# Performance work log

Measured on AMD Instinct MI355X. Metric: run time of the kernel, lower is better.

## Reference

```python
import jax, jax.numpy as jnp
import numpy as np

D_MODEL = 2816
N_HEADS = 16
DH = 512
N_KV = 2
MAX_CTX = 8192
POS = 4095  # current decode position (0-indexed)
EPS = 1e-6
Q_DIM = N_HEADS * DH
KV_DIM = N_KV * DH
NEG_INF = -1e9


def setup_inputs() -> dict:
    key = jax.random.key(0)
    ks = jax.random.split(key, 8)
    x = jax.random.normal(ks[0], (1, 1, D_MODEL), jnp.float32)
    # Realistic RoPE angles at position POS (full head_dim rotation, half/half layout)
    inv_freq = 1.0 / (10000.0 ** (np.arange(0, DH, 2, dtype=np.float32) / DH))  # (DH/2,)
    ang = POS * inv_freq
    cos = jnp.asarray(np.concatenate([np.cos(ang), np.cos(ang)])[None, None, :], jnp.float32)  # (1,1,DH)
    sin = jnp.asarray(np.concatenate([np.sin(ang), np.sin(ang)])[None, None, :], jnp.float32)
    k_cache = jax.random.normal(ks[1], (1, N_KV, MAX_CTX, DH), jnp.float32) * 0.02
    v_cache = jax.random.normal(ks[2], (1, N_KV, MAX_CTX, DH), jnp.float32) * 0.02
    # causal decode mask: attend to [0, POS], -inf beyond
    pos_ids = jnp.arange(MAX_CTX)
    attn_mask = jnp.where(pos_ids <= POS, 0.0, NEG_INF).astype(jnp.float32).reshape(1, 1, 1, MAX_CTX)
    # one-hot write mask at current position
    kv_write_mask = jnp.zeros((1, 1, MAX_CTX, 1), jnp.float32).at[0, 0, POS, 0].set(1.0)
    Wq = jax.random.normal(ks[3], (Q_DIM, D_MODEL), jnp.float32) * 0.02
    Wk = jax.random.normal(ks[4], (KV_DIM, D_MODEL), jnp.float32) * 0.02
    Wo = jax.random.normal(ks[5], (D_MODEL, Q_DIM), jnp.float32) * 0.02
    q_gamma = jax.random.normal(ks[6], (DH,), jnp.float32) * 0.02  # stored as (gamma-1)
    k_gamma = jax.random.normal(ks[7], (DH,), jnp.float32) * 0.02
    return {"x": x, "cos": cos, "sin": sin, "k_cache": k_cache, "v_cache": v_cache,
            "attn_mask": attn_mask, "kv_write_mask": kv_write_mask,
            "Wq": Wq, "Wk": Wk, "Wo": Wo, "q_gamma": q_gamma, "k_gamma": k_gamma}


def _rmsnorm(x, w=None):
    v = jnp.mean(x * x, axis=-1, keepdims=True)
    x = x * jax.lax.rsqrt(v + EPS)
    return x if w is None else x * (1.0 + w)


def _rope(x, cos, sin):
    # x: (1,T,H,D); cos/sin: (1,T,D)
    c = cos[:, :, None, :]
    s = sin[:, :, None, :]
    d = x.shape[-1]
    x1, x2 = x[..., : d // 2], x[..., d // 2 :]
    rot = jnp.concatenate([-x2, x1], axis=-1)
    return x * c + rot * s


def reference(x, cos, sin, k_cache, v_cache, attn_mask, kv_write_mask, Wq, Wk, Wo, q_gamma, k_gamma):
    q_raw = (x @ Wq.T).reshape(1, 1, N_HEADS, DH)
    k_raw = (x @ Wk.T).reshape(1, 1, N_KV, DH)
    q = _rope(_rmsnorm(q_raw, q_gamma), cos, sin)
    k = _rope(_rmsnorm(k_raw, k_gamma), cos, sin)
    v = _rmsnorm(k_raw)  # unscaled norm, not rotated
    q = jnp.swapaxes(q, 1, 2)  # (1,H,1,D)
    k = jnp.swapaxes(k, 1, 2)  # (1,n_kv,1,D)
    v = jnp.swapaxes(v, 1, 2)
    k_new = k_cache + k * kv_write_mask  # broadcast write at current slot
    v_new = v_cache + v * kv_write_mask
    rep = N_HEADS // N_KV
    K = jnp.repeat(k_new, rep, axis=1)  # (1,H,S,D)
    V = jnp.repeat(v_new, rep, axis=1)
    scores = jnp.einsum("bhtd,bhsd->bhts", q, K) + attn_mask  # no 1/sqrt(d) scale, as in source
    w = jax.nn.softmax(scores.astype(jnp.float32), axis=-1).astype(q.dtype)
    ctx = jnp.einsum("bhts,bhsd->bhtd", w, V)  # (1,H,1,D)
    ctx = jnp.swapaxes(ctx, 1, 2).reshape(1, 1, Q_DIM)
    out = ctx @ Wo.T
    return (out, k_new, v_new)
```

## Files before the change

kernel.cpp:

```cpp
#include <hip/hip_runtime.h>
#include <math.h>

#define D_MODEL 2816
#define N_HEADS 16
#define DH      512
#define N_KV    2
#define MAX_CTX 8192
#define POS     4095
#define EPS     1e-6f
#define Q_DIM   8192
#define KV_DIM  1024
#define GROUP   8
#define NPOS    4096
#define PV_CHUNK  64
#define PV_NCHUNK 64


__device__ __forceinline__ float4 f4_mul(float4 a, float s) {
  return make_float4(a.x*s, a.y*s, a.z*s, a.w*s);
}
__device__ __forceinline__ float4 f4_mul4(float4 a, float4 b) {
  return make_float4(a.x*b.x, a.y*b.y, a.z*b.z, a.w*b.w);
}
__device__ __forceinline__ float4 f4_fma(float4 a, float4 b, float4 c) {
  return make_float4(fmaf(a.x,b.x,c.x), fmaf(a.y,b.y,c.y), fmaf(a.z,b.z,c.z), fmaf(a.w,b.w,c.w));
}
__device__ __forceinline__ float4 f4_fnma(float4 a, float4 b, float4 c) {
  return make_float4(fmaf(-a.x,b.x,c.x), fmaf(-a.y,b.y,c.y), fmaf(-a.z,b.z,c.z), fmaf(-a.w,b.w,c.w));
}
__device__ __forceinline__ float4 f4_add(float4 a, float4 b) {
  return make_float4(a.x+b.x, a.y+b.y, a.z+b.z, a.w+b.w);
}
__device__ __forceinline__ float f4_dot(float4 a, float4 b) {
  return a.x*b.x + a.y*b.y + a.z*b.z + a.w*b.w;
}
__device__ __forceinline__ float f4_ssq(float4 a) {
  return a.x*a.x + a.y*a.y + a.z*a.z + a.w*a.w;
}

__global__ __launch_bounds__(256) void k_qkv(const float* __restrict__ x,
    const float* __restrict__ Wq, const float* __restrict__ Wk,
    float* __restrict__ qraw, float* __restrict__ kraw) {
  int wid  = (blockIdx.x * blockDim.x + threadIdx.x) >> 6;
  int lane = threadIdx.x & 63;
  const float4* x4 = (const float4*)x;
  int row = wid;
  const float4* W4 = (row < Q_DIM)
      ? (const float4*)(Wq + (size_t)row * D_MODEL)
      : (const float4*)(Wk + (size_t)(row - Q_DIM) * D_MODEL);
  float acc0 = 0.f, acc1 = 0.f;
#pragma unroll
  for (int it = 0; it < D_MODEL / 256; ++it) {
    float4 w  = W4[it * 64 + lane];
    float4 xv = x4[it * 64 + lane];
    float d = f4_dot(w, xv);
    if (it & 1) acc1 += d; else acc0 += d;
  }
  float acc = acc0 + acc1;
#pragma unroll
  for (int m = 32; m; m >>= 1) acc += __shfl_xor(acc, m, 64);
  if (lane == 0) {
    if (row < Q_DIM) qraw[row] = acc;
    else             kraw[row - Q_DIM] = acc;
  }
}

__global__ __launch_bounds__(512) void k_copy_scores(
    const float* __restrict__ kc, const float* __restrict__ vc,
    const float* __restrict__ qraw, const float* __restrict__ kraw,
    const float* __restrict__ cosv, const float* __restrict__ sinv,
    const float* __restrict__ qg,   const float* __restrict__ kg,
    float* __restrict__ knew, float* __restrict__ vnew,
    float* __restrict__ scores) {
  __shared__ float4 lq[GROUP * DH / 4];
  __shared__ float4 kfin[DH / 4];
  __shared__ float4 vfin[DH / 4];
  int b = blockIdx.x;
  int g = b >> 10;
  int t = threadIdx.x;
  int wid = t >> 6, lane = t & 63;

  const float4* c4 = (const float4*)cosv;
  const float4* s4 = (const float4*)sinv;
  float4 c1 = c4[lane],      s1 = s4[lane];
  float4 c2 = c4[64 + lane], s2 = s4[64 + lane];

  {
    const float4* qr4 = (const float4*)(qraw + (size_t)(g * GROUP + wid) * DH);
    float4 a  = qr4[lane];
    float4 b2 = qr4[64 + lane];
    float ss = f4_ssq(a) + f4_ssq(b2);
#pragma unroll
    for (int m = 32; m; m >>= 1) ss += __shfl_xor(ss, m, 64);
    float scale = rsqrtf(ss * (1.f / (float)DH) + EPS);
    const float4* qg4 = (const float4*)qg;
    float4 ga = qg4[lane], gb = qg4[64 + lane];
    float4 na = f4_mul4(f4_mul(a,  scale), make_float4(1.f+ga.x,1.f+ga.y,1.f+ga.z,1.f+ga.w));
    float4 nb = f4_mul4(f4_mul(b2, scale), make_float4(1.f+gb.x,1.f+gb.y,1.f+gb.z,1.f+gb.w));
    lq[wid * 128 + lane]      = f4_fnma(nb, s1, f4_mul4(na, c1));
    lq[wid * 128 + 64 + lane] = f4_fma (na, s2, f4_mul4(nb, c2));
  }

  bool has_pos = ((b & 1023) == (POS >> 3));
  if (has_pos && wid == 0) {
    const float4* kr4 = (const float4*)(kraw + (size_t)g * DH);
    float4 a  = kr4[lane];
    float4 b2 = kr4[64 + lane];
    float ss = f4_ssq(a) + f4_ssq(b2);
#pragma unroll
    for (int m = 32; m; m >>= 1) ss += __shfl_xor(ss, m, 64);
    float scale = rsqrtf(ss * (1.f / (float)DH) + EPS);
    float4 va_ = f4_mul(a,  scale);
    float4 vb_ = f4_mul(b2, scale);
    const float4* kg4 = (const float4*)kg;
    float4 ga = kg4[lane], gb = kg4[64 + lane];
    float4 na = f4_mul4(va_, make_float4(1.f+ga.x,1.f+ga.y,1.f+ga.z,1.f+ga.w));
    float4 nb = f4_mul4(vb_, make_float4(1.f+gb.x,1.f+gb.y,1.f+gb.z,1.f+gb.w));
    kfin[lane]      = f4_fnma(nb, s1, f4_mul4(na, c1));
    kfin[64 + lane] = f4_fma (na, s2, f4_mul4(nb, c2));
    vfin[lane]      = va_;
    vfin[64 + lane] = vb_;
  }
  __syncthreads();

  int s = ((b & 1023) << 3) + wid;
  size_t row = ((size_t)g * MAX_CTX + s) * DH;
  const float4* kc4 = (const float4*)(kc + row);
  const float4* vc4 = (const float4*)(vc + row);
  float4* ko4 = (float4*)(knew + row);
  float4* vo4 = (float4*)(vnew + row);
  float4 ka = kc4[lane], kb = kc4[64 + lane];
  float4 va = vc4[lane], vb = vc4[64 + lane];
  if (s == POS) {
    ka = f4_add(ka, kfin[lane]); kb = f4_add(kb, kfin[64 + lane]);
    va = f4_add(va, vfin[lane]); vb = f4_add(vb, vfin[64 + lane]);
  }
  ko4[lane] = ka; ko4[64 + lane] = kb;
  vo4[lane] = va; vo4[64 + lane] = vb;
  if (s <= POS) {
    float acc[GROUP];
#pragma unroll
    for (int h = 0; h < GROUP; ++h) {
      float4 qa = lq[h * 128 + lane], qb = lq[h * 128 + 64 + lane];
      acc[h] = f4_dot(qa, ka) + f4_dot(qb, kb);
    }
#pragma unroll
    for (int h = 0; h < GROUP; ++h) {
#pragma unroll
      for (int m = 32; m; m >>= 1) acc[h] += __shfl_xor(acc[h], m, 64);
    }
    if (lane == 0) {
#pragma unroll
      for (int h = 0; h < GROUP; ++h)
        scores[(size_t)(g * GROUP + h) * NPOS + s] = acc[h];
    }
  }
}

__global__ __launch_bounds__(512) void k_pv(
    const float* __restrict__ vnew, const float* __restrict__ scores,
    float* __restrict__ part, float* __restrict__ lpart) {
  __shared__ float lw[GROUP][PV_CHUNK];
  int b = blockIdx.x;
  int g = b >> 6;
  int c = b & (PV_NCHUNK - 1);
  int t = threadIdx.x;
  {
    int h = t >> 6, sl = t & 63;
    float sc = scores[(size_t)(g * GROUP + h) * NPOS + c * PV_CHUNK + sl];
    float e = __expf(fminf(sc, 80.f));
    lw[h][sl] = e;
    float le = e;
#pragma unroll
    for (int m = 32; m; m >>= 1) le += __shfl_xor(le, m, 64);
    if (sl == 0) lpart[(size_t)(g * PV_NCHUNK + c) * GROUP + h] = le;
  }
  __syncthreads();
  float acc[GROUP] = {0.f,0.f,0.f,0.f,0.f,0.f,0.f,0.f};
  for (int sl = 0; sl < PV_CHUNK; ++sl) {
    float vv = vnew[((size_t)g * MAX_CTX + c * PV_CHUNK + sl) * DH + t];
#pragma unroll
    for (int h = 0; h < GROUP; ++h) acc[h] = fmaf(lw[h][sl], vv, acc[h]);
  }
  float* p = part + (size_t)(g * PV_NCHUNK + c) * (GROUP * DH);
#pragma unroll
  for (int h = 0; h < GROUP; ++h) p[h * DH + t] = acc[h];
}

__global__ __launch_bounds__(256) void k_reduce_ctx(
    const float* __restrict__ part, const float* __restrict__ lpart,
    float* __restrict__ ctx) {
  int hd = blockIdx.x * 256 + threadIdx.x;
  int h = hd >> 9, d = hd & 511;
  int g = h >> 3, hh = h & 7;
  float acc = 0.f, l = 0.f;
  for (int c = 0; c < PV_NCHUNK; ++c) {
    acc += part[(size_t)(g * PV_NCHUNK + c) * (GROUP * DH) + hh * DH + d];
    l   += lpart[(size_t)(g * PV_NCHUNK + c) * GROUP + hh];
  }
  ctx[hd] = acc / l;
}

__global__ __launch_bounds__(256) void k_oproj(const float* __restrict__ ctx,
    const float* __restrict__ Wo, float* __restrict__ out) {
  int wid  = (blockIdx.x * blockDim.x + threadIdx.x) >> 6;
  int lane = threadIdx.x & 63;
  const float4* c4 = (const float4*)ctx;
  int row = wid;
  const float4* W4 = (const float4*)(Wo + (size_t)row * Q_DIM);
  float acc0 = 0.f, acc1 = 0.f;
#pragma unroll
  for (int it = 0; it < Q_DIM / 256; ++it) {
    float4 w  = W4[it * 64 + lane];
    float4 cv = c4[it * 64 + lane];
    float d = f4_dot(w, cv);
    if (it & 1) acc1 += d; else acc0 += d;
  }
  float acc = acc0 + acc1;
#pragma unroll
  for (int m = 32; m; m >>= 1) acc += __shfl_xor(acc, m, 64);
  if (lane == 0) out[row] = acc;
}

extern "C" void kernel_launch(void* const* d_in, const int* in_sizes, int n_in,
                              void* d_out, int out_size, void* d_ws, size_t ws_size,
                              hipStream_t stream) {
  (void)in_sizes; (void)n_in; (void)out_size; (void)ws_size;
  const float* x    = (const float*)d_in[0];
  const float* cosv = (const float*)d_in[1];
  const float* sinv = (const float*)d_in[2];
  const float* kc   = (const float*)d_in[3];
  const float* vc   = (const float*)d_in[4];
  const float* Wq   = (const float*)d_in[7];
  const float* Wk   = (const float*)d_in[8];
  const float* Wo   = (const float*)d_in[9];
  const float* qg   = (const float*)d_in[10];
  const float* kg   = (const float*)d_in[11];

  float* out  = (float*)d_out;
  float* knew = out + D_MODEL;
  float* vnew = knew + (size_t)N_KV * MAX_CTX * DH;

  float* w      = (float*)d_ws;
  float* qraw   = w;
  float* kraw   = w + 8192;
  float* scores = w + 9216;
  float* part   = w + 74752;
  float* lpart  = w + 599040;
  float* ctx    = w + 600064;

  k_qkv        <<<2304, 256, 0, stream>>>(x, Wq, Wk, qraw, kraw);
  k_copy_scores<<<2048, 512, 0, stream>>>(kc, vc, qraw, kraw, cosv, sinv, qg, kg,
                                          knew, vnew, scores);
  k_pv         <<<N_KV * PV_NCHUNK, 512, 0, stream>>>(vnew, scores, part, lpart);
  k_reduce_ctx <<<32, 256, 0, stream>>>(part, lpart, ctx);
  k_oproj      <<<704, 256, 0, stream>>>(ctx, Wo, out);
}
```

Before: 81.31 us.

## Fuse KV-cache copy, score computation and PV accumulation into one kernel

Merges the cache-copy/score kernel with the separate PV kernel. Each block now handles 32 consecutive positions, computes exp(score) and accumulates the weighted V values in registers while the K/V rows are already loaded. Per-block partials are reduced through shared memory. This removes the scores round trip and the second pass that re-read the new V cache from global memory. In exchange it launches fewer blocks (512), adds many __syncthreads in the partial reduction, and doubles the number of partials the reduce kernel must sum.

```diff
diff --git a/kernel.cpp b/kernel.cpp
--- a/kernel.cpp
+++ b/kernel.cpp
@@ -12,8 +12,7 @@
 #define KV_DIM  1024
 #define GROUP   8
 #define NPOS    4096
-#define PV_CHUNK  64
-#define PV_NCHUNK 64
+#define AB      128
 
 
 __device__ __forceinline__ float4 f4_mul(float4 a, float s) {
@@ -24,6 +23,9 @@
 }
 __device__ __forceinline__ float4 f4_fma(float4 a, float4 b, float4 c) {
   return make_float4(fmaf(a.x,b.x,c.x), fmaf(a.y,b.y,c.y), fmaf(a.z,b.z,c.z), fmaf(a.w,b.w,c.w));
+}
+__device__ __forceinline__ float4 f4_fmas(float s, float4 b, float4 c) {
+  return make_float4(fmaf(s,b.x,c.x), fmaf(s,b.y,c.y), fmaf(s,b.z,c.z), fmaf(s,b.w,c.w));
 }
 __device__ __forceinline__ float4 f4_fnma(float4 a, float4 b, float4 c) {
   return make_float4(fmaf(-a.x,b.x,c.x), fmaf(-a.y,b.y,c.y), fmaf(-a.z,b.z,c.z), fmaf(-a.w,b.w,c.w));
@@ -65,28 +67,31 @@
   }
 }
 
-__global__ __launch_bounds__(512) void k_copy_scores(
+__global__ __launch_bounds__(512) void k_fused(
     const float* __restrict__ kc, const float* __restrict__ vc,
     const float* __restrict__ qraw, const float* __restrict__ kraw,
     const float* __restrict__ cosv, const float* __restrict__ sinv,
     const float* __restrict__ qg,   const float* __restrict__ kg,
     float* __restrict__ knew, float* __restrict__ vnew,
-    float* __restrict__ scores) {
-  __shared__ float4 lq[GROUP * DH / 4];
-  __shared__ float4 kfin[DH / 4];
-  __shared__ float4 vfin[DH / 4];
+    float* __restrict__ part, float* __restrict__ lpart) {
+  __shared__ float4 lq[GROUP * 128];
+  __shared__ float  pvbuf[8 * 512];
+  __shared__ float  lbuf[64];
+  __shared__ float4 kfin[128];
+  __shared__ float4 vfin[128];
   int b = blockIdx.x;
-  int g = b >> 10;
+  int g = b >> 8;
+  int rb = b & 255;
   int t = threadIdx.x;
-  int wid = t >> 6, lane = t & 63;
-
-  const float4* c4 = (const float4*)cosv;
-  const float4* s4 = (const float4*)sinv;
-  float4 c1 = c4[lane],      s1 = s4[lane];
-  float4 c2 = c4[64 + lane], s2 = s4[64 + lane];
-
-  {
-    const float4* qr4 = (const float4*)(qraw + (size_t)(g * GROUP + wid) * DH);
+  int w = t >> 6, lane = t & 63;
+  bool att = (rb < AB);
+
+  if (att) {
+    const float4* c4 = (const float4*)cosv;
+    const float4* s4 = (const float4*)sinv;
+    float4 c1 = c4[lane],      s1 = s4[lane];
+    float4 c2 = c4[64 + lane], s2 = s4[64 + lane];
+    const float4* qr4 = (const float4*)(qraw + (size_t)(g * GROUP + w) * DH);
     float4 a  = qr4[lane];
     float4 b2 = qr4[64 + lane];
     float ss = f4_ssq(a) + f4_ssq(b2);
@@ -97,106 +102,109 @@
     float4 ga = qg4[lane], gb = qg4[64 + lane];
     float4 na = f4_mul4(f4_mul(a,  scale), make_float4(1.f+ga.x,1.f+ga.y,1.f+ga.z,1.f+ga.w));
     float4 nb = f4_mul4(f4_mul(b2, scale), make_float4(1.f+gb.x,1.f+gb.y,1.f+gb.z,1.f+gb.w));
-    lq[wid * 128 + lane]      = f4_fnma(nb, s1, f4_mul4(na, c1));
-    lq[wid * 128 + 64 + lane] = f4_fma (na, s2, f4_mul4(nb, c2));
-  }
-
-  bool has_pos = ((b & 1023) == (POS >> 3));
-  if (has_pos && wid == 0) {
-    const float4* kr4 = (const float4*)(kraw + (size_t)g * DH);
-    float4 a  = kr4[lane];
-    float4 b2 = kr4[64 + lane];
-    float ss = f4_ssq(a) + f4_ssq(b2);
-#pragma unroll
-    for (int m = 32; m; m >>= 1) ss += __shfl_xor(ss, m, 64);
-    float scale = rsqrtf(ss * (1.f / (float)DH) + EPS);
-    float4 va_ = f4_mul(a,  scale);
-    float4 vb_ = f4_mul(b2, scale);
-    const float4* kg4 = (const float4*)kg;
-    float4 ga = kg4[lane], gb = kg4[64 + lane];
-    float4 na = f4_mul4(va_, make_float4(1.f+ga.x,1.f+ga.y,1.f+ga.z,1.f+ga.w));
-    float4 nb = f4_mul4(vb_, make_float4(1.f+gb.x,1.f+gb.y,1.f+gb.z,1.f+gb.w));
-    kfin[lane]      = f4_fnma(nb, s1, f4_mul4(na, c1));
-    kfin[64 + lane] = f4_fma (na, s2, f4_mul4(nb, c2));
-    vfin[lane]      = va_;
-    vfin[64 + lane] = vb_;
+    lq[w * 128 + lane]      = f4_fnma(nb, s1, f4_mul4(na, c1));
+    lq[w * 128 + 64 + lane] = f4_fma (na, s2, f4_mul4(nb, c2));
+    if (rb == (POS >> 5) && w == 0) {
+      const float4* kr4 = (const float4*)(kraw + (size_t)g * DH);
+      float4 ka_ = kr4[lane];
+      float4 kb_ = kr4[64 + lane];
+      float ss2 = f4_ssq(ka_) + f4_ssq(kb_);
+#pragma unroll
+      for (int m = 32; m; m >>= 1) ss2 += __shfl_xor(ss2, m, 64);
+      float sc2 = rsqrtf(ss2 * (1.f / (float)DH) + EPS);
+      float4 va_ = f4_mul(ka_, sc2);
+      float4 vb_ = f4_mul(kb_, sc2);
+      const float4* kg4 = (const float4*)kg;
+      float4 ga2 = kg4[lane], gb2 = kg4[64 + lane];
+      float4 na2 = f4_mul4(va_, make_float4(1.f+ga2.x,1.f+ga2.y,1.f+ga2.z,1.f+ga2.w));
+      float4 nb2 = f4_mul4(vb_, make_float4(1.f+gb2.x,1.f+gb2.y,1.f+gb2.z,1.f+gb2.w));
+      kfin[lane]      = f4_fnma(nb2, s1, f4_mul4(na2, c1));
+      kfin[64 + lane] = f4_fma (na2, s2, f4_mul4(nb2, c2));
+      vfin[lane]      = va_;
+      vfin[64 + lane] = vb_;
+    }
   }
   __syncthreads();
 
-  int s = ((b & 1023) << 3) + wid;
-  size_t row = ((size_t)g * MAX_CTX + s) * DH;
-  const float4* kc4 = (const float4*)(kc + row);
-  const float4* vc4 = (const float4*)(vc + row);
-  float4* ko4 = (float4*)(knew + row);
-  float4* vo4 = (float4*)(vnew + row);
-  float4 ka = kc4[lane], kb = kc4[64 + lane];
-  float4 va = vc4[lane], vb = vc4[64 + lane];
-  if (s == POS) {
-    ka = f4_add(ka, kfin[lane]); kb = f4_add(kb, kfin[64 + lane]);
-    va = f4_add(va, vfin[lane]); vb = f4_add(vb, vfin[64 + lane]);
-  }
-  ko4[lane] = ka; ko4[64 + lane] = kb;
-  vo4[lane] = va; vo4[64 + lane] = vb;
-  if (s <= POS) {
-    float acc[GROUP];
+  float4 acc[GROUP][2];
+#pragma unroll
+  for (int h = 0; h < GROUP; ++h) { acc[h][0] = make_float4(0,0,0,0); acc[h][1] = make_float4(0,0,0,0); }
+  float lacc[GROUP] = {0.f,0.f,0.f,0.f,0.f,0.f,0.f,0.f};
+
+  for (int r = 0; r < 4; ++r) {
+    int s = (rb << 5) + (w << 2) + r;
+    size_t row = ((size_t)g * MAX_CTX + s) * DH;
+    const float4* kc4 = (const float4*)(kc + row);
+    const float4* vc4 = (const float4*)(vc + row);
+    float4 ka = kc4[lane], kb = kc4[64 + lane];
+    float4 va = vc4[lane], vb = vc4[64 + lane];
+    if (s == POS) {
+      ka = f4_add(ka, kfin[lane]); kb = f4_add(kb, kfin[64 + lane]);
+      va = f4_add(va, vfin[lane]); vb = f4_add(vb, vfin[64 + lane]);
+    }
+    float4* ko4 = (float4*)(knew + row);
+    float4* vo4 = (float4*)(vnew + row);
+    ko4[lane] = ka; ko4[64 + lane] = kb;
+    vo4[lane] = va; vo4[64 + lane] = vb;
+    if (att) {
+      float sc[GROUP];
+#pragma unroll
+      for (int h = 0; h < GROUP; ++h)
+        sc[h] = f4_dot(lq[h * 128 + lane], ka) + f4_dot(lq[h * 128 + 64 + lane], kb);
+#pragma unroll
+      for (int h = 0; h < GROUP; ++h) {
+#pragma unroll
+        for (int m = 32; m; m >>= 1) sc[h] += __shfl_xor(sc[h], m, 64);
+      }
+#pragma unroll
+      for (int h = 0; h < GROUP; ++h) {
+        float e = __expf(fminf(sc[h], 80.f));
+        lacc[h] += e;
+        acc[h][0] = f4_fmas(e, va, acc[h][0]);
+        acc[h][1] = f4_fmas(e, vb, acc[h][1]);
+      }
+    }
+  }
+
+  if (att) {
+    float4* pv4 = (float4*)pvbuf;
 #pragma unroll
     for (int h = 0; h < GROUP; ++h) {
-      float4 qa = lq[h * 128 + lane], qb = lq[h * 128 + 64 + lane];
-      acc[h] = f4_dot(qa, ka) + f4_dot(qb, kb);
-    }
-#pragma unroll
-    for (int h = 0; h < GROUP; ++h) {
-#pragma unroll
-      for (int m = 32; m; m >>= 1) acc[h] += __shfl_xor(acc[h], m, 64);
-    }
-    if (lane == 0) {
-#pragma unroll
-      for (int h = 0; h < GROUP; ++h)
-        scores[(size_t)(g * GROUP + h) * NPOS + s] = acc[h];
-    }
-  }
-}
-
-__global__ __launch_bounds__(512) void k_pv(
-    const float* __restrict__ vnew, const float* __restrict__ scores,
-    float* __restrict__ part, float* __restrict__ lpart) {
-  __shared__ float lw[GROUP][PV_CHUNK];
-  int b = blockIdx.x;
-  int g = b >> 6;
-  int c = b & (PV_NCHUNK - 1);
-  int t = threadIdx.x;
-  {
-    int h = t >> 6, sl = t & 63;
-    float sc = scores[(size_t)(g * GROUP + h) * NPOS + c * PV_CHUNK + sl];
-    float e = __expf(fminf(sc, 80.f));
-    lw[h][sl] = e;
-    float le = e;
-#pragma unroll
-    for (int m = 32; m; m >>= 1) le += __shfl_xor(le, m, 64);
-    if (sl == 0) lpart[(size_t)(g * PV_NCHUNK + c) * GROUP + h] = le;
-  }
-  __syncthreads();
-  float acc[GROUP] = {0.f,0.f,0.f,0.f,0.f,0.f,0.f,0.f};
-  for (int sl = 0; sl < PV_CHUNK; ++sl) {
-    float vv = vnew[((size_t)g * MAX_CTX + c * PV_CHUNK + sl) * DH + t];
-#pragma unroll
-    for (int h = 0; h < GROUP; ++h) acc[h] = fmaf(lw[h][sl], vv, acc[h]);
-  }
-  float* p = part + (size_t)(g * PV_NCHUNK + c) * (GROUP * DH);
-#pragma unroll
-  for (int h = 0; h < GROUP; ++h) p[h * DH + t] = acc[h];
+      __syncthreads();
+      pv4[w * 128 + lane]      = acc[h][0];
+      pv4[w * 128 + 64 + lane] = acc[h][1];
+      __syncthreads();
+      float sum = 0.f;
+#pragma unroll
+      for (int w2 = 0; w2 < 8; ++w2) sum += pvbuf[w2 * 512 + t];
+      part[((size_t)(g * AB + rb)) * (GROUP * DH) + h * 512 + t] = sum;
+    }
+    float myl = 0.f;
+#pragma unroll
+    for (int h = 0; h < GROUP; ++h) myl = (lane == h) ? lacc[h] : myl;
+    if (lane < 8) lbuf[w * 8 + lane] = myl;
+    __syncthreads();
+    if (t < 8) {
+      float sl = 0.f;
+#pragma unroll
+      for (int w2 = 0; w2 < 8; ++w2) sl += lbuf[w2 * 8 + t];
+      lpart[(g * AB + rb) * 8 + t] = sl;
+    }
+  }
 }
 
 __global__ __launch_bounds__(256) void k_reduce_ctx(
     const float* __restrict__ part, const float* __restrict__ lpart,
     float* __restrict__ ctx) {
   int hd = blockIdx.x * 256 + threadIdx.x;
-  int h = hd >> 9, d = hd & 511;
+  int h = hd >> 9;
   int g = h >> 3, hh = h & 7;
+  const float* p  = part  + (size_t)g * AB * (GROUP * DH) + hh * 512 + (hd & 511);
+  const float* lp = lpart + g * AB * 8 + hh;
   float acc = 0.f, l = 0.f;
-  for (int c = 0; c < PV_NCHUNK; ++c) {
-    acc += part[(size_t)(g * PV_NCHUNK + c) * (GROUP * DH) + hh * DH + d];
-    l   += lpart[(size_t)(g * PV_NCHUNK + c) * GROUP + hh];
+  for (int c = 0; c < AB; ++c) {
+    acc += p[(size_t)c * (GROUP * DH)];
+    l   += lp[c * 8];
   }
   ctx[hd] = acc / l;
 }
@@ -244,15 +252,13 @@
   float* w      = (float*)d_ws;
   float* qraw   = w;
   float* kraw   = w + 8192;
-  float* scores = w + 9216;
-  float* part   = w + 74752;
-  float* lpart  = w + 599040;
-  float* ctx    = w + 600064;
-
-  k_qkv        <<<2304, 256, 0, stream>>>(x, Wq, Wk, qraw, kraw);
-  k_copy_scores<<<2048, 512, 0, stream>>>(kc, vc, qraw, kraw, cosv, sinv, qg, kg,
-                                          knew, vnew, scores);
-  k_pv         <<<N_KV * PV_NCHUNK, 512, 0, stream>>>(vnew, scores, part, lpart);
-  k_reduce_ctx <<<32, 256, 0, stream>>>(part, lpart, ctx);
-  k_oproj      <<<704, 256, 0, stream>>>(ctx, Wo, out);
-}
+  float* part   = w + 9216;
+  float* lpart  = w + 1057792;
+  float* ctx    = w + 1059840;
+
+  k_qkv       <<<2304, 256, 0, stream>>>(x, Wq, Wk, qraw, kraw);
+  k_fused     <<<512, 512, 0, stream>>>(kc, vc, qraw, kraw, cosv, sinv, qg, kg,
+                                        knew, vnew, part, lpart);
+  k_reduce_ctx<<<32, 256, 0, stream>>>(part, lpart, ctx);
+  k_oproj     <<<704, 256, 0, stream>>>(ctx, Wo, out);
+}
```

Result: faster. 79.18 us (-2.6%).
